# Performance work log

Measured on AMD Instinct MI355X. Metric: run time of the kernel, lower is better.

## Reference

```python
import jax, jax.numpy as jnp
import numpy as np
import math

EPS = 1.1920929e-07  # torch.finfo(float32).eps, used by nn.RMSNorm when eps=None
N_HEADS = 16

def _rmsnorm(x, w):
    return x * jax.lax.rsqrt(jnp.mean(x * x, axis=-1, keepdims=True) + EPS) * w

def setup_inputs() -> dict:
    key = jax.random.key(0)
    D, V, FF = 1024, 32000, 2048
    NS, IPS = 4, 8
    B, T = 2, 1024
    ks = jax.random.split(key, 8)
    sd = 0.02
    g = lambda i, shape: jax.random.normal(ks[i], shape, jnp.float32) * sd
    return {
        "tokens": jax.random.randint(ks[0], (B, T), 0, V),
        "embed_w": g(1, (V, D)),
        "qkv_w": g(2, (3 * D, D)),
        "o_w": g(3, (D, D)),
        "gate_w": g(4, (FF, D)),
        "up_w": g(5, (FF, D)),
        "down_w": g(6, (D, FF)),
        "norm1_w": jnp.ones((D,), jnp.float32),
        "norm2_w": jnp.ones((D,), jnp.float32),
        "scale_gamma": jnp.ones((NS, D), jnp.float32),
        "scale_beta": jnp.zeros((NS, D), jnp.float32),
        "iter_scale": jnp.ones((NS, IPS), jnp.float32),
        "norm_w": jnp.ones((D,), jnp.float32),
        "lm_head_w": g(7, (V, D)),
    }

def _block(x, gamma, beta, qkv_w, o_w, gate_w, up_w, down_w, norm1_w, norm2_w):
    B, T, D = x.shape
    hd = D // N_HEADS
    # pre-attn norm + FiLM modulation
    h = _rmsnorm(x, norm1_w) * gamma + beta
    qkv = (h @ qkv_w.T).reshape(B, T, 3, N_HEADS, hd)
    q = jnp.transpose(qkv[:, :, 0], (0, 2, 1, 3))  # [B,H,T,hd]
    k = jnp.transpose(qkv[:, :, 1], (0, 2, 1, 3))
    v = jnp.transpose(qkv[:, :, 2], (0, 2, 1, 3))
    scores = jnp.einsum('bhqd,bhkd->bhqk', q, k) / math.sqrt(hd)
    causal = jnp.tril(jnp.ones((T, T), dtype=bool))
    scores = jnp.where(causal, scores, -jnp.inf)
    attn = jax.nn.softmax(scores, axis=-1)
    out = jnp.einsum('bhqk,bhkd->bhqd', attn, v)
    out = jnp.transpose(out, (0, 2, 1, 3)).reshape(B, T, D)
    x = x + out @ o_w.T
    # pre-FFN norm + FiLM modulation, SwiGLU
    h2 = _rmsnorm(x, norm2_w) * gamma + beta
    x = x + (jax.nn.silu(h2 @ gate_w.T) * (h2 @ up_w.T)) @ down_w.T
    return x

def reference(tokens, embed_w, qkv_w, o_w, gate_w, up_w, down_w, norm1_w,
              norm2_w, scale_gamma, scale_beta, iter_scale, norm_w, lm_head_w):
    NS, IPS = iter_scale.shape
    x = embed_w[tokens].astype(jnp.float32)  # [B,T,D]
    # flatten (scale, iter) schedule to per-virtual-layer params [NS*IPS, ...]
    gammas = jnp.repeat(scale_gamma, IPS, axis=0)
    betas = jnp.repeat(scale_beta, IPS, axis=0)
    iters = iter_scale.reshape(-1)

    @jax.checkpoint
    def step(x, per):
        g, b, s = per
        y = _block(x, g, b, qkv_w, o_w, gate_w, up_w, down_w, norm1_w, norm2_w)
        return x + (y - x) * s, None

    x, _ = jax.lax.scan(step, x, (gammas, betas, iters))
    return _rmsnorm(x, norm_w) @ lm_head_w.T  # [B,T,V]
```

## Files before the change

### kernel.cpp

```cpp
#include <hip/hip_runtime.h>

typedef __bf16 bf16;
typedef __attribute__((ext_vector_type(8))) __bf16 bf16x8;
typedef __attribute__((ext_vector_type(4))) __bf16 bf16x4;
typedef __attribute__((ext_vector_type(4))) float f32x4;

#define MFMA16(a,b,c) __builtin_amdgcn_mfma_f32_16x16x32_bf16((a),(b),(c),0,0,0)

__device__ __forceinline__ void gload16(const void* g, void* l) {
    __builtin_amdgcn_global_load_lds((const __attribute__((address_space(1))) void*)g,
                                     (__attribute__((address_space(3))) void*)l, 16, 0, 0);
}


__global__ __launch_bounds__(256) void cvt_kernel(const float* __restrict__ in,
                                                  bf16* __restrict__ out, int n4) {
    int stride = gridDim.x * 256;
    for (int i = blockIdx.x * 256 + threadIdx.x; i < n4; i += stride) {
        float4 v = ((const float4*)in)[i];
        bf16x4 o;
        o[0] = (bf16)v.x; o[1] = (bf16)v.y; o[2] = (bf16)v.z; o[3] = (bf16)v.w;
        ((bf16x4*)out)[i] = o;
    }
}

__global__ __launch_bounds__(256) void embed_kernel(const int* __restrict__ tok,
                                                    const float* __restrict__ ew,
                                                    float* __restrict__ X) {
    int m = blockIdx.x;
    int t = tok[m];
    ((float4*)(X + (size_t)m * 1024))[threadIdx.x] =
        ((const float4*)(ew + (size_t)t * 1024))[threadIdx.x];
}

template <bool FILM>
__global__ __launch_bounds__(256) void rmsnorm_kernel(const float* __restrict__ X,
                                                      const float* __restrict__ w,
                                                      const float* __restrict__ gamma,
                                                      const float* __restrict__ beta,
                                                      bf16* __restrict__ H) {
    int m = blockIdx.x, t = threadIdx.x;
    float4 xv = ((const float4*)(X + (size_t)m * 1024))[t];
    float ss = xv.x * xv.x + xv.y * xv.y + xv.z * xv.z + xv.w * xv.w;
#pragma unroll
    for (int off = 1; off < 64; off <<= 1) ss += __shfl_xor(ss, off);
    __shared__ float red[4];
    if ((t & 63) == 0) red[t >> 6] = ss;
    __syncthreads();
    float tot = red[0] + red[1] + red[2] + red[3];
    float sc = rsqrtf(tot * (1.0f / 1024.0f) + 1.1920929e-07f);
    float4 wv = ((const float4*)w)[t];
    float r0 = xv.x * sc * wv.x, r1 = xv.y * sc * wv.y;
    float r2 = xv.z * sc * wv.z, r3 = xv.w * sc * wv.w;
    if (FILM) {
        float4 gv = ((const float4*)gamma)[t];
        float4 bv = ((const float4*)beta)[t];
        r0 = r0 * gv.x + bv.x; r1 = r1 * gv.y + bv.y;
        r2 = r2 * gv.z + bv.z; r3 = r3 * gv.w + bv.w;
    }
    bf16x4 o;
    o[0] = (bf16)r0; o[1] = (bf16)r1; o[2] = (bf16)r2; o[3] = (bf16)r3;
    ((bf16x4*)(H + (size_t)m * 1024))[t] = o;
}


template <int MT, int MODE>
__global__ __launch_bounds__(256, 2) void gemm_bt(const bf16* __restrict__ A,
                                                  const bf16* __restrict__ B,
                                                  int N, int K,
                                                  bf16* __restrict__ Cb, float* __restrict__ Cf,
                                                  const float* __restrict__ Xin,
                                                  const float* __restrict__ Xin2,
                                                  float* __restrict__ Xout,
                                                  const float* __restrict__ sptr) {
    constexpr int BM = 32 * MT;
    __shared__ __align__(16) bf16 As[BM * 64];
    __shared__ __align__(16) bf16 Bs[128 * 64];
    const int bn = blockIdx.x, bm = blockIdx.y;
    const int tid = threadIdx.x, lane = tid & 63, w = tid >> 6;
    const int wr = w >> 1, wc = w & 1, lr = lane & 15, lg = lane >> 4;
    const bf16* Ab = A + (size_t)bm * BM * K;
    const bf16* Bb = B + (size_t)bn * 128 * K;

    f32x4 acc[MT][4];
#pragma unroll
    for (int i = 0; i < MT; ++i)
#pragma unroll
        for (int j = 0; j < 4; ++j) acc[i][j] = (f32x4){0.f, 0.f, 0.f, 0.f};

    for (int kt = 0; kt < K; kt += 64) {
        __syncthreads();
#pragma unroll
        for (int i = 0; i < MT; ++i) {
            int cw = i * 256 + w * 64;
            int cid = cw + lane;
            gload16(Ab + (size_t)(cid >> 3) * K + kt + (cid & 7) * 8, As + cw * 8);
        }
#pragma unroll
        for (int i = 0; i < 4; ++i) {
            int cw = i * 256 + w * 64;
            int cid = cw + lane;
            gload16(Bb + (size_t)(cid >> 3) * K + kt + (cid & 7) * 8, Bs + cw * 8);
        }
        __syncthreads();
#pragma unroll
        for (int kk = 0; kk < 64; kk += 32) {
            bf16x8 af[MT], bfr[4];
#pragma unroll
            for (int mi = 0; mi < MT; ++mi)
                af[mi] = *(const bf16x8*)(As + (wr * (16 * MT) + mi * 16 + lr) * 64 + kk + lg * 8);
#pragma unroll
            for (int ni = 0; ni < 4; ++ni)
                bfr[ni] = *(const bf16x8*)(Bs + (wc * 64 + ni * 16 + lr) * 64 + kk + lg * 8);
#pragma unroll
            for (int mi = 0; mi < MT; ++mi)
#pragma unroll
                for (int ni = 0; ni < 4; ++ni)
                    acc[mi][ni] = MFMA16(af[mi], bfr[ni], acc[mi][ni]);
        }
    }

    float s1 = (MODE == 2) ? sptr[0] : 0.f;
#pragma unroll
    for (int mi = 0; mi < MT; ++mi) {
#pragma unroll
        for (int ni = 0; ni < 4; ++ni) {
#pragma unroll
            for (int j = 0; j < 4; ++j) {
                int row = bm * BM + wr * (16 * MT) + mi * 16 + lg * 4 + j;
                int col = bn * 128 + wc * 64 + ni * 16 + lr;
                size_t idx = (size_t)row * N + col;
                float v = acc[mi][ni][j];
                if (MODE == 0) Cb[idx] = (bf16)v;
                else if (MODE == 1) Xout[idx] = Xin[idx] + v;
                else if (MODE == 2) Xout[idx] = Xin[idx] + s1 * (Xin2[idx] - Xin[idx] + v);
                else Cf[idx] = v;
            }
        }
    }
}


__global__ __launch_bounds__(256, 2) void gemm_gateup(const bf16* __restrict__ A,
                                                      const bf16* __restrict__ Bg,
                                                      const bf16* __restrict__ Bu,
                                                      bf16* __restrict__ FF) {
    const int K = 1024, N = 2048;
    __shared__ __align__(16) bf16 As[128 * 64];
    __shared__ __align__(16) bf16 Gs[128 * 64];
    __shared__ __align__(16) bf16 Us[128 * 64];
    const int bn = blockIdx.x, bm = blockIdx.y;
    const int tid = threadIdx.x, lane = tid & 63, w = tid >> 6;
    const int wr = w >> 1, wc = w & 1, lr = lane & 15, lg = lane >> 4;
    const bf16* Ab = A + (size_t)bm * 128 * K;
    const bf16* Gb = Bg + (size_t)bn * 128 * K;
    const bf16* Ub = Bu + (size_t)bn * 128 * K;

    f32x4 ag[4][4], au[4][4];
#pragma unroll
    for (int i = 0; i < 4; ++i)
#pragma unroll
        for (int j = 0; j < 4; ++j) {
            ag[i][j] = (f32x4){0.f, 0.f, 0.f, 0.f};
            au[i][j] = (f32x4){0.f, 0.f, 0.f, 0.f};
        }

    for (int kt = 0; kt < K; kt += 64) {
        __syncthreads();
#pragma unroll
        for (int i = 0; i < 4; ++i) {
            int cw = i * 256 + w * 64;
            int cid = cw + lane;
            size_t ro = (size_t)(cid >> 3) * K + kt + (cid & 7) * 8;
            gload16(Ab + ro, As + cw * 8);
            gload16(Gb + ro, Gs + cw * 8);
            gload16(Ub + ro, Us + cw * 8);
        }
        __syncthreads();
#pragma unroll
        for (int kk = 0; kk < 64; kk += 32) {
            bf16x8 af[4], gf[4], uf[4];
#pragma unroll
            for (int mi = 0; mi < 4; ++mi)
                af[mi] = *(const bf16x8*)(As + (wr * 64 + mi * 16 + lr) * 64 + kk + lg * 8);
#pragma unroll
            for (int ni = 0; ni < 4; ++ni) {
                gf[ni] = *(const bf16x8*)(Gs + (wc * 64 + ni * 16 + lr) * 64 + kk + lg * 8);
                uf[ni] = *(const bf16x8*)(Us + (wc * 64 + ni * 16 + lr) * 64 + kk + lg * 8);
            }
#pragma unroll
            for (int mi = 0; mi < 4; ++mi)
#pragma unroll
                for (int ni = 0; ni < 4; ++ni) {
                    ag[mi][ni] = MFMA16(af[mi], gf[ni], ag[mi][ni]);
                    au[mi][ni] = MFMA16(af[mi], uf[ni], au[mi][ni]);
                }
        }
    }

#pragma unroll
    for (int mi = 0; mi < 4; ++mi) {
#pragma unroll
        for (int ni = 0; ni < 4; ++ni) {
#pragma unroll
            for (int j = 0; j < 4; ++j) {
                int row = bm * 128 + wr * 64 + mi * 16 + lg * 4 + j;
                int col = bn * 128 + wc * 64 + ni * 16 + lr;
                float g = ag[mi][ni][j], u = au[mi][ni][j];
                float sg = g / (1.0f + __expf(-g));
                FF[(size_t)row * N + col] = (bf16)(sg * u);
            }
        }
    }
}


__global__ __launch_bounds__(256) void attn_kernel(const bf16* __restrict__ QKV,
                                                   bf16* __restrict__ AO) {
    const int qt = blockIdx.x, bh = blockIdx.y;
    const int b = bh >> 4, h = bh & 15;
    const int tid = threadIdx.x;
    const int w = tid >> 6, lane = tid & 63;
    const int lr = lane & 15, lg = lane >> 4;

    __shared__ __align__(16) bf16 Ks[64 * 72];
    __shared__ __align__(16) bf16 Vt[64 * 72];
    __shared__ __align__(16) bf16 Ps[4 * 16 * 72];
    bf16* Pw = Ps + w * 16 * 72;

    const int qrow = b * 1024 + qt * 64 + w * 16 + lr;
    const bf16* qptr = QKV + (size_t)qrow * 3072 + h * 64;
    bf16x8 qf0 = *(const bf16x8*)(qptr + lg * 8);
    bf16x8 qf1 = *(const bf16x8*)(qptr + 32 + lg * 8);

    f32x4 o[4];
#pragma unroll
    for (int i = 0; i < 4; ++i) o[i] = (f32x4){0.f, 0.f, 0.f, 0.f};
    float m_run = -1e30f, l_run = 0.f;
    const int gq = qt * 64 + w * 16 + lr;

    for (int kt = 0; kt <= qt; ++kt) {
        __syncthreads();
#pragma unroll
        for (int i = 0; i < 2; ++i) {
            int cid = tid + 256 * i;
            int r = cid >> 3, c8 = (cid & 7) * 8;
            const bf16* kvrow = QKV + (size_t)(b * 1024 + kt * 64 + r) * 3072 + h * 64;
            *(bf16x8*)(Ks + r * 72 + c8) = *(const bf16x8*)(kvrow + 1024 + c8);
            bf16x8 vv = *(const bf16x8*)(kvrow + 2048 + c8);
#pragma unroll
            for (int ii = 0; ii < 8; ++ii) Vt[(c8 + ii) * 72 + r] = vv[ii];
        }
        __syncthreads();

        f32x4 st[4];
#pragma unroll
        for (int i = 0; i < 4; ++i) st[i] = (f32x4){0.f, 0.f, 0.f, 0.f};
#pragma unroll
        for (int ki = 0; ki < 4; ++ki) {
            bf16x8 kf0 = *(const bf16x8*)(Ks + (ki * 16 + lr) * 72 + lg * 8);
            bf16x8 kf1 = *(const bf16x8*)(Ks + (ki * 16 + lr) * 72 + 32 + lg * 8);
            st[ki] = MFMA16(kf0, qf0, st[ki]);
            st[ki] = MFMA16(kf1, qf1, st[ki]);
        }
        bool diag = (kt == qt);
        float pm = -1e30f;
#pragma unroll
        for (int ki = 0; ki < 4; ++ki) {
#pragma unroll
            for (int j = 0; j < 4; ++j) {
                float sv = st[ki][j] * 0.125f;
                if (diag) {
                    int gk = kt * 64 + ki * 16 + lg * 4 + j;
                    if (gk > gq) sv = -1e30f;
                }
                st[ki][j] = sv;
                pm = fmaxf(pm, sv);
            }
        }
        pm = fmaxf(pm, __shfl_xor(pm, 16));
        pm = fmaxf(pm, __shfl_xor(pm, 32));
        float m_new = fmaxf(m_run, pm);
        float alpha = __expf(m_run - m_new);
        float rs = 0.f;
#pragma unroll
        for (int ki = 0; ki < 4; ++ki) {
            bf16x4 pb;
#pragma unroll
            for (int j = 0; j < 4; ++j) {
                float pv = __expf(st[ki][j] - m_new);
                rs += pv;
                pb[j] = (bf16)pv;
            }
            *(bf16x4*)(Pw + lr * 72 + ki * 16 + lg * 4) = pb;
        }
        rs += __shfl_xor(rs, 16);
        rs += __shfl_xor(rs, 32);
        l_run = l_run * alpha + rs;
        m_run = m_new;
#pragma unroll
        for (int di = 0; di < 4; ++di) o[di] *= alpha;
#pragma unroll
        for (int dk = 0; dk < 2; ++dk) {
            bf16x8 pf = *(const bf16x8*)(Pw + lr * 72 + dk * 32 + lg * 8);
#pragma unroll
            for (int di = 0; di < 4; ++di) {
                bf16x8 vf = *(const bf16x8*)(Vt + (di * 16 + lr) * 72 + dk * 32 + lg * 8);
                o[di] = MFMA16(vf, pf, o[di]);
            }
        }
    }
    float inv = 1.0f / l_run;
    bf16* optr = AO + (size_t)qrow * 1024 + h * 64;
#pragma unroll
    for (int di = 0; di < 4; ++di) {
        bf16x4 ov;
#pragma unroll
        for (int j = 0; j < 4; ++j) ov[j] = (bf16)(o[di][j] * inv);
        *(bf16x4*)(optr + di * 16 + lg * 4) = ov;
    }
}


extern "C" void kernel_launch(void* const* d_in, const int* in_sizes, int n_in,
                              void* d_out, int out_size, void* d_ws, size_t ws_size,
                              hipStream_t stream) {
    const int* tokens = (const int*)d_in[0];
    const float* embed_w = (const float*)d_in[1];
    const float* qkv_w = (const float*)d_in[2];
    const float* o_w = (const float*)d_in[3];
    const float* gate_w = (const float*)d_in[4];
    const float* up_w = (const float*)d_in[5];
    const float* down_w = (const float*)d_in[6];
    const float* norm1_w = (const float*)d_in[7];
    const float* norm2_w = (const float*)d_in[8];
    const float* scale_gamma = (const float*)d_in[9];
    const float* scale_beta = (const float*)d_in[10];
    const float* iter_scale = (const float*)d_in[11];
    const float* norm_w = (const float*)d_in[12];
    const float* lm_head_w = (const float*)d_in[13];

    char* p = (char*)d_ws;
    auto alloc = [&](size_t nbytes) -> char* {
        char* r = p;
        p += (nbytes + 255) & ~(size_t)255;
        return r;
    };
    bf16* WQKV = (bf16*)alloc(3072ull * 1024 * 2);
    bf16* WO   = (bf16*)alloc(1024ull * 1024 * 2);
    bf16* WG   = (bf16*)alloc(2048ull * 1024 * 2);
    bf16* WU   = (bf16*)alloc(2048ull * 1024 * 2);
    bf16* WD   = (bf16*)alloc(1024ull * 2048 * 2);
    bf16* WLM  = (bf16*)alloc(32000ull * 1024 * 2);
    float* X   = (float*)alloc(2048ull * 1024 * 4);
    float* X1  = (float*)alloc(2048ull * 1024 * 4);
    bf16* H    = (bf16*)alloc(2048ull * 1024 * 2);
    bf16* QKVb = (bf16*)alloc(2048ull * 3072 * 2);
    bf16* AO   = (bf16*)alloc(2048ull * 1024 * 2);
    bf16* FF   = (bf16*)alloc(2048ull * 2048 * 2);

    cvt_kernel<<<1024, 256, 0, stream>>>(qkv_w, WQKV, 3072 * 1024 / 4);
    cvt_kernel<<<1024, 256, 0, stream>>>(o_w, WO, 1024 * 1024 / 4);
    cvt_kernel<<<1024, 256, 0, stream>>>(gate_w, WG, 2048 * 1024 / 4);
    cvt_kernel<<<1024, 256, 0, stream>>>(up_w, WU, 2048 * 1024 / 4);
    cvt_kernel<<<1024, 256, 0, stream>>>(down_w, WD, 1024 * 2048 / 4);
    cvt_kernel<<<2048, 256, 0, stream>>>(lm_head_w, WLM, 32000 * 1024 / 4);
    embed_kernel<<<2048, 256, 0, stream>>>(tokens, embed_w, X);

    for (int l = 0; l < 32; ++l) {
        const float* gm = scale_gamma + (size_t)(l >> 3) * 1024;
        const float* bt = scale_beta + (size_t)(l >> 3) * 1024;
        rmsnorm_kernel<true><<<2048, 256, 0, stream>>>(X, norm1_w, gm, bt, H);
        gemm_bt<4, 0><<<dim3(24, 16), 256, 0, stream>>>(H, WQKV, 3072, 1024,
                                                        QKVb, nullptr, nullptr, nullptr, nullptr, nullptr);
        attn_kernel<<<dim3(16, 32), 256, 0, stream>>>(QKVb, AO);
        gemm_bt<2, 1><<<dim3(8, 32), 256, 0, stream>>>(AO, WO, 1024, 1024,
                                                       nullptr, nullptr, X, nullptr, X1, nullptr);
        rmsnorm_kernel<true><<<2048, 256, 0, stream>>>(X1, norm2_w, gm, bt, H);
        gemm_gateup<<<dim3(16, 16), 256, 0, stream>>>(H, WG, WU, FF);
        gemm_bt<2, 2><<<dim3(8, 32), 256, 0, stream>>>(FF, WD, 1024, 2048,
                                                       nullptr, nullptr, X, X1, X, iter_scale + l);
    }
    rmsnorm_kernel<false><<<2048, 256, 0, stream>>>(X, norm_w, nullptr, nullptr, H);
    gemm_bt<4, 3><<<dim3(250, 16), 256, 0, stream>>>(H, WLM, 32000, 1024,
                                                     nullptr, (float*)d_out, nullptr, nullptr, nullptr, nullptr);
}
```

Measured before the change: 5.424 ms.

## Swizzle GEMM workgroup order across XCDs and raise MFMA priority in attention

GEMM launches become 1D grids, and each workgroup remaps its ID with an XCD-aware swizzle. Tiles that share A or B operands then run on the same XCD and reuse its L2 cache. The attention kernel also wraps its MFMA sections in s_setprio so matrix work is favoured over other waves. The remapping adds some integer arithmetic per block, and the priority hints may or may not help scheduling.

```diff
diff --git a/kernel.cpp b/kernel.cpp
--- a/kernel.cpp
+++ b/kernel.cpp
@@ -10,6 +10,13 @@
 __device__ __forceinline__ void gload16(const void* g, void* l) {
     __builtin_amdgcn_global_load_lds((const __attribute__((address_space(1))) void*)g,
                                      (__attribute__((address_space(3))) void*)l, 16, 0, 0);
+}
+
+__device__ __forceinline__ int xcd_swizzle(int orig, int nwg) {
+    int q = nwg >> 3, r = nwg & 7;
+    int xcd = orig & 7, loc = orig >> 3;
+    int base = (xcd < r) ? xcd * (q + 1) : r * (q + 1) + (xcd - r) * q;
+    return base + loc;
 }
 
 
@@ -64,9 +71,10 @@
 }
 
 
-template <int MT, int MODE>
+template <int MT, int MODE, bool BNF>
 __global__ __launch_bounds__(256, 2) void gemm_bt(const bf16* __restrict__ A,
                                                   const bf16* __restrict__ B,
+                                                  int GN, int GM,
                                                   int N, int K,
                                                   bf16* __restrict__ Cb, float* __restrict__ Cf,
                                                   const float* __restrict__ Xin,
@@ -76,7 +84,10 @@
     constexpr int BM = 32 * MT;
     __shared__ __align__(16) bf16 As[BM * 64];
     __shared__ __align__(16) bf16 Bs[128 * 64];
-    const int bn = blockIdx.x, bm = blockIdx.y;
+    const int wg = xcd_swizzle(blockIdx.x, GN * GM);
+    int bn, bm;
+    if (BNF) { bm = wg / GN; bn = wg - bm * GN; }
+    else     { bn = wg / GM; bm = wg - bn * GM; }
     const int tid = threadIdx.x, lane = tid & 63, w = tid >> 6;
     const int wr = w >> 1, wc = w & 1, lr = lane & 15, lg = lane >> 4;
     const bf16* Ab = A + (size_t)bm * BM * K;
@@ -149,7 +160,8 @@
     __shared__ __align__(16) bf16 As[128 * 64];
     __shared__ __align__(16) bf16 Gs[128 * 64];
     __shared__ __align__(16) bf16 Us[128 * 64];
-    const int bn = blockIdx.x, bm = blockIdx.y;
+    const int wg = xcd_swizzle(blockIdx.x, 256);
+    const int bn = wg >> 4, bm = wg & 15;
     const int tid = threadIdx.x, lane = tid & 63, w = tid >> 6;
     const int wr = w >> 1, wc = w & 1, lr = lane & 15, lg = lane >> 4;
     const bf16* Ab = A + (size_t)bm * 128 * K;
@@ -256,6 +268,7 @@
         f32x4 st[4];
 #pragma unroll
         for (int i = 0; i < 4; ++i) st[i] = (f32x4){0.f, 0.f, 0.f, 0.f};
+        __builtin_amdgcn_s_setprio(1);
 #pragma unroll
         for (int ki = 0; ki < 4; ++ki) {
             bf16x8 kf0 = *(const bf16x8*)(Ks + (ki * 16 + lr) * 72 + lg * 8);
@@ -263,6 +276,7 @@
             st[ki] = MFMA16(kf0, qf0, st[ki]);
             st[ki] = MFMA16(kf1, qf1, st[ki]);
         }
+        __builtin_amdgcn_s_setprio(0);
         bool diag = (kt == qt);
         float pm = -1e30f;
 #pragma unroll
@@ -300,6 +314,7 @@
         m_run = m_new;
 #pragma unroll
         for (int di = 0; di < 4; ++di) o[di] *= alpha;
+        __builtin_amdgcn_s_setprio(1);
 #pragma unroll
         for (int dk = 0; dk < 2; ++dk) {
             bf16x8 pf = *(const bf16x8*)(Pw + lr * 72 + dk * 32 + lg * 8);
@@ -309,6 +324,7 @@
                 o[di] = MFMA16(vf, pf, o[di]);
             }
         }
+        __builtin_amdgcn_s_setprio(0);
     }
     float inv = 1.0f / l_run;
     bf16* optr = AO + (size_t)qrow * 1024 + h * 64;
@@ -371,17 +387,17 @@
         const float* gm = scale_gamma + (size_t)(l >> 3) * 1024;
         const float* bt = scale_beta + (size_t)(l >> 3) * 1024;
         rmsnorm_kernel<true><<<2048, 256, 0, stream>>>(X, norm1_w, gm, bt, H);
-        gemm_bt<4, 0><<<dim3(24, 16), 256, 0, stream>>>(H, WQKV, 3072, 1024,
-                                                        QKVb, nullptr, nullptr, nullptr, nullptr, nullptr);
+        gemm_bt<4, 0, false><<<24 * 16, 256, 0, stream>>>(H, WQKV, 24, 16, 3072, 1024,
+                                                          QKVb, nullptr, nullptr, nullptr, nullptr, nullptr);
         attn_kernel<<<dim3(16, 32), 256, 0, stream>>>(QKVb, AO);
-        gemm_bt<2, 1><<<dim3(8, 32), 256, 0, stream>>>(AO, WO, 1024, 1024,
-                                                       nullptr, nullptr, X, nullptr, X1, nullptr);
+        gemm_bt<2, 1, true><<<8 * 32, 256, 0, stream>>>(AO, WO, 8, 32, 1024, 1024,
+                                                        nullptr, nullptr, X, nullptr, X1, nullptr);
         rmsnorm_kernel<true><<<2048, 256, 0, stream>>>(X1, norm2_w, gm, bt, H);
-        gemm_gateup<<<dim3(16, 16), 256, 0, stream>>>(H, WG, WU, FF);
-        gemm_bt<2, 2><<<dim3(8, 32), 256, 0, stream>>>(FF, WD, 1024, 2048,
-                                                       nullptr, nullptr, X, X1, X, iter_scale + l);
+        gemm_gateup<<<256, 256, 0, stream>>>(H, WG, WU, FF);
+        gemm_bt<2, 2, true><<<8 * 32, 256, 0, stream>>>(FF, WD, 8, 32, 1024, 2048,
+                                                        nullptr, nullptr, X, X1, X, iter_scale + l);
     }
     rmsnorm_kernel<false><<<2048, 256, 0, stream>>>(X, norm_w, nullptr, nullptr, H);
-    gemm_bt<4, 3><<<dim3(250, 16), 256, 0, stream>>>(H, WLM, 32000, 1024,
-                                                     nullptr, (float*)d_out, nullptr, nullptr, nullptr, nullptr);
-}
+    gemm_bt<4, 3, false><<<250 * 16, 256, 0, stream>>>(H, WLM, 250, 16, 32000, 1024,
+                                                       nullptr, (float*)d_out, nullptr, nullptr, nullptr, nullptr);
+}
```

New measurement: 5.282 ms. -2.6%, faster.
